# Kernel tuning notes

Measured on AMD Instinct MI355X. Metric: run time of the kernel, lower is better.

Reference implementation:

```python
import jax, jax.numpy as jnp
import numpy as np

NUM_DEPTH_BINS = 64
EPS = 1e-8


def bilinear_grid_sample(feats, grid):
    """torch.nn.functional.grid_sample, mode='bilinear', padding_mode='zeros',
    align_corners=False.  feats: [N, C, H, W]; grid: [N, Ho, Wo, 2] in [-1, 1].
    Returns [N, C, Ho, Wo]."""
    N, C, H, W = feats.shape
    x = (grid[..., 0] + 1.0) * (W * 0.5) - 0.5  # [N, Ho, Wo]
    y = (grid[..., 1] + 1.0) * (H * 0.5) - 0.5
    x0 = jnp.floor(x)
    y0 = jnp.floor(y)
    wx1 = x - x0
    wy1 = y - y0
    wx0 = 1.0 - wx1
    wy0 = 1.0 - wy1
    feats_flat = feats.reshape(N, C, H * W)

    def gather(ix, iy):
        valid = (ix >= 0) & (ix <= W - 1) & (iy >= 0) & (iy <= H - 1)
        ixc = jnp.clip(ix, 0, W - 1).astype(jnp.int32)
        iyc = jnp.clip(iy, 0, H - 1).astype(jnp.int32)
        idx = (iyc * W + ixc).reshape(N, 1, -1)  # [N,1,Ho*Wo]
        f = jnp.take_along_axis(feats_flat, idx, axis=2).reshape(N, C, *ix.shape[1:])
        return f * valid[:, None].astype(feats.dtype)

    out = (gather(x0, y0) * (wx0 * wy0)[:, None]
           + gather(x0 + 1, y0) * (wx1 * wy0)[:, None]
           + gather(x0, y0 + 1) * (wx0 * wy1)[:, None]
           + gather(x0 + 1, y0 + 1) * (wx1 * wy1)[:, None])
    return out


def _cost_volume(cur_feats, src_feats, src_extrinsics, src_Ks, cur_invK, min_depth, max_depth):
    B, K, C, H, W = src_feats.shape
    D = NUM_DEPTH_BINS
    # log-spaced depth planes, shape [B, D, 1, 1]
    ramp = jnp.linspace(0.0, 1.0, D).reshape(1, D, 1, 1).astype(cur_feats.dtype)
    depth_planes_bd11 = jnp.exp(jnp.log(min_depth) + jnp.log(max_depth / min_depth) * ramp)
    # BackprojectDepth: half-pixel-centered homogeneous pixel coords [3, N]
    xs, ys = jnp.meshgrid(jnp.arange(W, dtype=cur_feats.dtype) + 0.5,
                          jnp.arange(H, dtype=cur_feats.dtype) + 0.5)
    pix_3n = jnp.stack([xs.ravel(), ys.ravel(), jnp.ones(H * W, cur_feats.dtype)])
    cam_dirs_b3n = jnp.einsum('bij,jn->bin', cur_invK[:, :3, :3], pix_3n)
    world_bd3n = depth_planes_bd11.reshape(B, D, 1, 1) * cam_dirs_b3n[:, None]  # [B,D,3,N]
    world_bd4n = jnp.concatenate(
        [world_bd3n, jnp.ones((B, D, 1, H * W), world_bd3n.dtype)], axis=2)
    # Project3D: P = K @ extrinsics, project, perspective divide
    P_bk34 = jnp.einsum('bkij,bkjl->bkil', src_Ks, src_extrinsics)[:, :, :3]
    cam_bkd3n = jnp.einsum('bkij,bdjn->bkdin', P_bk34, world_bd4n)  # [B,K,D,3,N]
    z_bkdn = cam_bkd3n[:, :, :, 2]
    pix_bkd2n = cam_bkd3n[:, :, :, :2] / (z_bkdn[:, :, :, None] + EPS)
    # uv = 2 * pix * (1/W, 1/H) - 1
    u = 2.0 * pix_bkd2n[:, :, :, 0] / W - 1.0
    v = 2.0 * pix_bkd2n[:, :, :, 1] / H - 1.0
    grid = jnp.stack([u, v], axis=-1).reshape(B * K, D * H, W, 2)
    warped = bilinear_grid_sample(src_feats.reshape(B * K, C, H, W), grid)
    warped = warped.reshape(B, K, C, D, H, W)
    mask = (z_bkdn > 0).astype(cur_feats.dtype).reshape(B, K, D, H, W)
    # channel dot product with current features, masked, summed over views
    dots_bkdhw = jnp.einsum('bkcdhw,bchw->bkdhw', warped, cur_feats) * mask
    cost_volume_bdhw = dots_bkdhw.sum(axis=1)
    return cost_volume_bdhw


def setup_inputs() -> dict:
    key = jax.random.key(0)
    B, K, C, H, W = 1, 7, 16, 96, 128
    k1, k2 = jax.random.split(key)
    cur_feats = jax.random.normal(k1, (B, C, H, W), jnp.float32)
    src_feats = jax.random.normal(k2, (B, K, C, H, W), jnp.float32)
    rng = np.random.default_rng(0)
    fx = 0.8 * W
    Kmat = np.array([[fx, 0, W / 2, 0], [0, fx, H / 2, 0],
                     [0, 0, 1, 0], [0, 0, 0, 1]], np.float32)

    def small_pose():
        aa = rng.normal(size=3) * 0.05
        th = np.linalg.norm(aa)
        ax = aa / (th + 1e-12)
        Kx = np.array([[0, -ax[2], ax[1]], [ax[2], 0, -ax[0]], [-ax[1], ax[0], 0]])
        R = np.eye(3) + np.sin(th) * Kx + (1 - np.cos(th)) * (Kx @ Kx)
        T = np.eye(4, dtype=np.float64)
        T[:3, :3] = R
        T[:3, 3] = rng.normal(size=3) * 0.08
        return T

    src_extrinsics = np.stack([[small_pose() for _ in range(K)] for _ in range(B)])
    src_poses = np.linalg.inv(src_extrinsics)
    return {
        'cur_feats': cur_feats,
        'src_feats': src_feats,
        'src_extrinsics': jnp.asarray(src_extrinsics, jnp.float32),
        'src_poses': jnp.asarray(src_poses, jnp.float32),
        'src_Ks': jnp.asarray(np.broadcast_to(Kmat, (B, K, 4, 4)).copy()),
        'cur_invK': jnp.asarray(np.broadcast_to(np.linalg.inv(Kmat), (B, 4, 4)).astype(np.float32).copy()),
        'min_depth': jnp.full((B, 1, 1, 1), 0.25, jnp.float32),
        'max_depth': jnp.full((B, 1, 1, 1), 5.0, jnp.float32),
    }


def reference(cur_feats, src_feats, src_extrinsics, src_poses, src_Ks, cur_invK, min_depth, max_depth):
    del src_poses  # unused, matching the original (del src_poses)
    return _cost_volume(cur_feats, src_feats, src_extrinsics, src_Ks, cur_invK, min_depth, max_depth)
```

## Files before the change

kernel.cpp:

```cpp
#include <hip/hip_runtime.h>

#define CV_H 96
#define CV_W 128
#define CV_C 16
#define CV_K 7
#define CV_D 64
#define CV_EPS 1e-8f
#define CV_HW (CV_H * CV_W)

typedef _Float16 v2h __attribute__((ext_vector_type(2)));
typedef _Float16 v8h __attribute__((ext_vector_type(8)));

#if __has_builtin(__builtin_amdgcn_fdot2)
#define FDOT2(a, b, c) __builtin_amdgcn_fdot2((a), (b), (c), false)
#else
#define FDOT2(a, b, c) ((float)(a)[0] * (float)(b)[0] + (float)(a)[1] * (float)(b)[1] + (c))
#endif

__global__ __launch_bounds__(256) void cv_prep(
    const float* __restrict__ cur, const float* __restrict__ src,
    const float* __restrict__ extr, const float* __restrict__ Ks,
    const float* __restrict__ invK, const float* __restrict__ minD,
    const float* __restrict__ maxD,
    float* __restrict__ depths, float* __restrict__ M,
    _Float16* __restrict__ srcT, _Float16* __restrict__ curT) {
    const int b = blockIdx.x;
    if (b == (CV_K + 1) * CV_H) {
        int t = threadIdx.x;
        if (t < CV_D) {
            float mn = minD[0], mx = maxD[0];
            float ramp = (float)t * (1.0f / (CV_D - 1));
            depths[t] = expf(logf(mn) + logf(mx / mn) * ramp);
        }
        if (t < CV_K) {
            const float* Km = Ks + t * 16;
            const float* E  = extr + t * 16;
            float P[3][4];
            for (int i = 0; i < 3; ++i)
                for (int j = 0; j < 4; ++j) {
                    float s = 0.f;
                    for (int l = 0; l < 4; ++l) s += Km[i * 4 + l] * E[l * 4 + j];
                    P[i][j] = s;
                }
            float* Mk = M + t * 12;
            for (int i = 0; i < 3; ++i)
                for (int j = 0; j < 3; ++j) {
                    float s = 0.f;
                    for (int l = 0; l < 3; ++l) s += P[i][l] * invK[l * 4 + j];
                    Mk[i * 3 + j] = s;
                }
            for (int i = 0; i < 3; ++i) Mk[9 + i] = P[i][3];
        }
        return;
    }
    const int g = b / CV_H;
    const int h = b % CV_H;
    const float* rowBase = (g < CV_K) ? (src + (size_t)g * CV_C * CV_HW + h * CV_W)
                                      : (cur + h * CV_W);
    __shared__ float lds[CV_C][CV_W + 2];
    const int t = threadIdx.x;
#pragma unroll
    for (int i = 0; i < 2; ++i) {
        int f  = t + i * 256;
        int c  = f >> 5;
        int w4 = (f & 31) << 2;
        float4 v = *(const float4*)(rowBase + (size_t)c * CV_HW + w4);
        lds[c][w4 + 0] = v.x; lds[c][w4 + 1] = v.y;
        lds[c][w4 + 2] = v.z; lds[c][w4 + 3] = v.w;
    }
    __syncthreads();
    const int p  = t >> 1;
    const int cb = (t & 1) << 3;
    v8h o;
#pragma unroll
    for (int j = 0; j < 8; ++j) o[j] = (_Float16)lds[cb + j][p];
    _Float16* dst = (g < CV_K)
        ? (srcT + ((size_t)g * CV_HW + h * CV_W + p) * CV_C + cb)
        : (curT + ((size_t)h * CV_W + p) * CV_C + cb);
    *(v8h*)dst = o;
}

__device__ __forceinline__ float dot16h(v8h a0, v8h a1, v8h b0, v8h b1) {
    const v2h* pa0 = (const v2h*)&a0; const v2h* pb0 = (const v2h*)&b0;
    const v2h* pa1 = (const v2h*)&a1; const v2h* pb1 = (const v2h*)&b1;
    float s = 0.f;
#pragma unroll
    for (int i = 0; i < 4; ++i) s = FDOT2(pa0[i], pb0[i], s);
#pragma unroll
    for (int i = 0; i < 4; ++i) s = FDOT2(pa1[i], pb1[i], s);
    return s;
}

__global__ __launch_bounds__(256, 4) void cv_main(
    const _Float16* __restrict__ srcT,
    const _Float16* __restrict__ curT,
    const float* __restrict__ depths,
    const float* __restrict__ Mg,
    float* __restrict__ out) {
    const int bx = blockIdx.x;
    const int wb = bx & 15;
    const int hb = (bx >> 4) % 12;
    const int db = bx / 192;
    const int wx = threadIdx.x & 7;
    const int hy = (threadIdx.x >> 3) & 7;
    const int dd = threadIdx.x >> 6;
    const int w = wb * 8 + wx;
    const int h = hb * 8 + hy;
    const int d = db * 4 + dd;

    const float px = w + 0.5f;
    const float py = h + 0.5f;
    const float depth = depths[d];

    const v8h* cp = (const v8h*)(curT + (h * CV_W + w) * CV_C);
    const v8h c0 = cp[0], c1 = cp[1];

    float acc = 0.f;
#pragma unroll
    for (int k = 0; k < CV_K; ++k) {
        const float* Mk = Mg + k * 12;
        float qx = Mk[0] * px + Mk[1] * py + Mk[2];
        float qy = Mk[3] * px + Mk[4] * py + Mk[5];
        float qz = Mk[6] * px + Mk[7] * py + Mk[8];
        float cx = depth * qx + Mk[9];
        float cy = depth * qy + Mk[10];
        float cz = depth * qz + Mk[11];
        float valid = (cz > 0.f) ? 1.f : 0.f;
        float inv = 1.0f / (fabsf(cz) + CV_EPS);
        float x = fminf(fmaxf(cx * inv - 0.5f, -4.0f), (float)(CV_W + 3));
        float y = fminf(fmaxf(cy * inv - 0.5f, -4.0f), (float)(CV_H + 3));
        float xf = floorf(x), yf = floorf(y);
        float wx1 = x - xf, wy1 = y - yf;
        float wx0 = 1.f - wx1, wy0 = 1.f - wy1;
        int x0 = (int)xf, y0 = (int)yf;
        int x1 = x0 + 1, y1 = y0 + 1;
        bool vx0 = (unsigned)x0 < (unsigned)CV_W;
        bool vx1 = (unsigned)x1 < (unsigned)CV_W;
        bool vy0 = (unsigned)y0 < (unsigned)CV_H;
        bool vy1 = (unsigned)y1 < (unsigned)CV_H;
        int cx0 = min(max(x0, 0), CV_W - 1);
        int cx1 = min(max(x1, 0), CV_W - 1);
        int cy0 = min(max(y0, 0), CV_H - 1);
        int cy1 = min(max(y1, 0), CV_H - 1);
        const v8h* base = (const v8h*)srcT + (size_t)k * (CV_HW * 2);
        const v8h* r0 = base + cy0 * (CV_W * 2);
        const v8h* r1 = base + cy1 * (CV_W * 2);
        v8h a00 = r0[cx0 * 2], b00 = r0[cx0 * 2 + 1];
        v8h a10 = r0[cx1 * 2], b10 = r0[cx1 * 2 + 1];
        v8h a01 = r1[cx0 * 2], b01 = r1[cx0 * 2 + 1];
        v8h a11 = r1[cx1 * 2], b11 = r1[cx1 * 2 + 1];
        float w00 = (vx0 && vy0) ? wx0 * wy0 : 0.f;
        float w10 = (vx1 && vy0) ? wx1 * wy0 : 0.f;
        float w01 = (vx0 && vy1) ? wx0 * wy1 : 0.f;
        float w11 = (vx1 && vy1) ? wx1 * wy1 : 0.f;
        float s = w00 * dot16h(a00, b00, c0, c1)
                + w10 * dot16h(a10, b10, c0, c1)
                + w01 * dot16h(a01, b01, c0, c1)
                + w11 * dot16h(a11, b11, c0, c1);
        acc = fmaf(valid, s, acc);
    }
    out[(d * CV_H + h) * CV_W + w] = acc;
}

extern "C" void kernel_launch(void* const* d_in, const int* in_sizes, int n_in,
                              void* d_out, int out_size, void* d_ws, size_t ws_size,
                              hipStream_t stream) {
    const float* cur_feats = (const float*)d_in[0];
    const float* src_feats = (const float*)d_in[1];
    const float* extr      = (const float*)d_in[2];
    const float* Ks        = (const float*)d_in[4];
    const float* invK      = (const float*)d_in[5];
    const float* minD      = (const float*)d_in[6];
    const float* maxD      = (const float*)d_in[7];
    float* out = (float*)d_out;

    float* wsf    = (float*)d_ws;
    float* depths = wsf;
    float* M      = wsf + 64;
    _Float16* srcT = (_Float16*)(wsf + 256);
    _Float16* curT = srcT + CV_K * CV_HW * CV_C;

    cv_prep<<<(CV_K + 1) * CV_H + 1, 256, 0, stream>>>(
        cur_feats, src_feats, extr, Ks, invK, minD, maxD, depths, M, srcT, curT);

    cv_main<<<CV_D / 4 * (CV_H / 8) * (CV_W / 8), 256, 0, stream>>>(
        srcT, curT, depths, M, out);
}
```

Before: 34.30 us.

## Fuse prep and main kernels with a grid-wide atomic barrier

Merges the transpose/convert prep kernel and the cost-volume kernel into one 768-block launch. Blocks first transpose their feature rows to fp16, then wait on a global atomic counter barrier before sampling. Each thread now handles 4 depth planes so projection terms are reused across them. Each block also recomputes the projection matrices and depth values itself. The aim is to drop a kernel launch gap, at the cost of a memset, a spin barrier that needs all 768 blocks co-resident, and redundant per-block setup.

```diff
diff --git a/kernel.cpp b/kernel.cpp
--- a/kernel.cpp
+++ b/kernel.cpp
@@ -7,6 +7,7 @@
 #define CV_D 64
 #define CV_EPS 1e-8f
 #define CV_HW (CV_H * CV_W)
+#define CV_NBLK 768
 
 typedef _Float16 v2h __attribute__((ext_vector_type(2)));
 typedef _Float16 v8h __attribute__((ext_vector_type(8)));
@@ -16,69 +17,6 @@
 #else
 #define FDOT2(a, b, c) ((float)(a)[0] * (float)(b)[0] + (float)(a)[1] * (float)(b)[1] + (c))
 #endif
-
-__global__ __launch_bounds__(256) void cv_prep(
-    const float* __restrict__ cur, const float* __restrict__ src,
-    const float* __restrict__ extr, const float* __restrict__ Ks,
-    const float* __restrict__ invK, const float* __restrict__ minD,
-    const float* __restrict__ maxD,
-    float* __restrict__ depths, float* __restrict__ M,
-    _Float16* __restrict__ srcT, _Float16* __restrict__ curT) {
-    const int b = blockIdx.x;
-    if (b == (CV_K + 1) * CV_H) {
-        int t = threadIdx.x;
-        if (t < CV_D) {
-            float mn = minD[0], mx = maxD[0];
-            float ramp = (float)t * (1.0f / (CV_D - 1));
-            depths[t] = expf(logf(mn) + logf(mx / mn) * ramp);
-        }
-        if (t < CV_K) {
-            const float* Km = Ks + t * 16;
-            const float* E  = extr + t * 16;
-            float P[3][4];
-            for (int i = 0; i < 3; ++i)
-                for (int j = 0; j < 4; ++j) {
-                    float s = 0.f;
-                    for (int l = 0; l < 4; ++l) s += Km[i * 4 + l] * E[l * 4 + j];
-                    P[i][j] = s;
-                }
-            float* Mk = M + t * 12;
-            for (int i = 0; i < 3; ++i)
-                for (int j = 0; j < 3; ++j) {
-                    float s = 0.f;
-                    for (int l = 0; l < 3; ++l) s += P[i][l] * invK[l * 4 + j];
-                    Mk[i * 3 + j] = s;
-                }
-            for (int i = 0; i < 3; ++i) Mk[9 + i] = P[i][3];
-        }
-        return;
-    }
-    const int g = b / CV_H;
-    const int h = b % CV_H;
-    const float* rowBase = (g < CV_K) ? (src + (size_t)g * CV_C * CV_HW + h * CV_W)
-                                      : (cur + h * CV_W);
-    __shared__ float lds[CV_C][CV_W + 2];
-    const int t = threadIdx.x;
-#pragma unroll
-    for (int i = 0; i < 2; ++i) {
-        int f  = t + i * 256;
-        int c  = f >> 5;
-        int w4 = (f & 31) << 2;
-        float4 v = *(const float4*)(rowBase + (size_t)c * CV_HW + w4);
-        lds[c][w4 + 0] = v.x; lds[c][w4 + 1] = v.y;
-        lds[c][w4 + 2] = v.z; lds[c][w4 + 3] = v.w;
-    }
-    __syncthreads();
-    const int p  = t >> 1;
-    const int cb = (t & 1) << 3;
-    v8h o;
-#pragma unroll
-    for (int j = 0; j < 8; ++j) o[j] = (_Float16)lds[cb + j][p];
-    _Float16* dst = (g < CV_K)
-        ? (srcT + ((size_t)g * CV_HW + h * CV_W + p) * CV_C + cb)
-        : (curT + ((size_t)h * CV_W + p) * CV_C + cb);
-    *(v8h*)dst = o;
-}
 
 __device__ __forceinline__ float dot16h(v8h a0, v8h a1, v8h b0, v8h b1) {
     const v2h* pa0 = (const v2h*)&a0; const v2h* pb0 = (const v2h*)&b0;
@@ -91,75 +29,146 @@
     return s;
 }
 
-__global__ __launch_bounds__(256, 4) void cv_main(
-    const _Float16* __restrict__ srcT,
-    const _Float16* __restrict__ curT,
-    const float* __restrict__ depths,
-    const float* __restrict__ Mg,
-    float* __restrict__ out) {
-    const int bx = blockIdx.x;
-    const int wb = bx & 15;
-    const int hb = (bx >> 4) % 12;
-    const int db = bx / 192;
-    const int wx = threadIdx.x & 7;
-    const int hy = (threadIdx.x >> 3) & 7;
-    const int dd = threadIdx.x >> 6;
-    const int w = wb * 8 + wx;
-    const int h = hb * 8 + hy;
-    const int d = db * 4 + dd;
+__global__ __launch_bounds__(256, 4) void cv_fused(
+    const float* __restrict__ cur, const float* __restrict__ src,
+    const float* __restrict__ extr, const float* __restrict__ Ks,
+    const float* __restrict__ invK, const float* __restrict__ minD,
+    const float* __restrict__ maxD,
+    _Float16* __restrict__ srcT, _Float16* __restrict__ curT,
+    unsigned* __restrict__ counter, float* __restrict__ out) {
+    const int b = blockIdx.x;
+    const int t = threadIdx.x;
+
+    __shared__ float Ml[CV_K][12];
+    __shared__ float dparams[2];
+
+    {
+        const int g = b / CV_H, h = b % CV_H;
+        const float* rowBase = (g < CV_K) ? src + (size_t)g * CV_C * CV_HW + h * CV_W
+                                          : cur + h * CV_W;
+        __shared__ float lds[CV_C][CV_W + 2];
+#pragma unroll
+        for (int i = 0; i < 2; ++i) {
+            int f = t + i * 256, c = f >> 5, w4 = (f & 31) << 2;
+            float4 v = *(const float4*)(rowBase + (size_t)c * CV_HW + w4);
+            lds[c][w4 + 0] = v.x; lds[c][w4 + 1] = v.y;
+            lds[c][w4 + 2] = v.z; lds[c][w4 + 3] = v.w;
+        }
+        __syncthreads();
+        int p = t >> 1, cb = (t & 1) << 3;
+        v8h o;
+#pragma unroll
+        for (int j = 0; j < 8; ++j) o[j] = (_Float16)lds[cb + j][p];
+        _Float16* dst = (g < CV_K)
+            ? (srcT + ((size_t)g * CV_HW + h * CV_W + p) * CV_C + cb)
+            : (curT + ((size_t)h * CV_W + p) * CV_C + cb);
+        *(v8h*)dst = o;
+    }
+
+    if (t < CV_K * 12) {
+        int k = t / 12, e = t % 12;
+        const float* Km = Ks + k * 16;
+        const float* E  = extr + k * 16;
+        float s = 0.f;
+        if (e < 9) {
+            int i = e / 3, j = e % 3;
+            for (int l = 0; l < 3; ++l) {
+                float P = 0.f;
+                for (int m = 0; m < 4; ++m) P += Km[i * 4 + m] * E[m * 4 + l];
+                s += P * invK[l * 4 + j];
+            }
+        } else {
+            int i = e - 9;
+            for (int m = 0; m < 4; ++m) s += Km[i * 4 + m] * E[m * 4 + 3];
+        }
+        Ml[k][e] = s;
+    }
+    if (t == 255) {
+        float mn = minD[0], mx = maxD[0];
+        dparams[0] = logf(mn);
+        dparams[1] = logf(mx / mn);
+    }
+
+    __syncthreads();
+    if (t == 0) {
+        __threadfence();
+        atomicAdd(counter, 1u);
+        while (atomicAdd(counter, 0u) < CV_NBLK) {
+            __builtin_amdgcn_s_sleep(2);
+        }
+        __threadfence();
+    }
+    __syncthreads();
+
+    const int wx = t & 7, hy = (t >> 3) & 7, dd = t >> 6;
+    const int rem = b % 192;
+    const int db2 = b / 192;
+    const int w = (rem & 15) * 8 + wx;
+    const int h = (rem >> 4) * 8 + hy;
+    const int dbase = db2 * 16 + dd * 4;
 
     const float px = w + 0.5f;
     const float py = h + 0.5f;
-    const float depth = depths[d];
+    const float ld = dparams[0], lr = dparams[1];
+    float dpt[4];
+#pragma unroll
+    for (int j = 0; j < 4; ++j)
+        dpt[j] = expf(ld + lr * ((float)(dbase + j) * (1.0f / 63.0f)));
 
     const v8h* cp = (const v8h*)(curT + (h * CV_W + w) * CV_C);
     const v8h c0 = cp[0], c1 = cp[1];
 
-    float acc = 0.f;
+    float acc[4] = {0.f, 0.f, 0.f, 0.f};
 #pragma unroll
     for (int k = 0; k < CV_K; ++k) {
-        const float* Mk = Mg + k * 12;
-        float qx = Mk[0] * px + Mk[1] * py + Mk[2];
-        float qy = Mk[3] * px + Mk[4] * py + Mk[5];
-        float qz = Mk[6] * px + Mk[7] * py + Mk[8];
-        float cx = depth * qx + Mk[9];
-        float cy = depth * qy + Mk[10];
-        float cz = depth * qz + Mk[11];
-        float valid = (cz > 0.f) ? 1.f : 0.f;
-        float inv = 1.0f / (fabsf(cz) + CV_EPS);
-        float x = fminf(fmaxf(cx * inv - 0.5f, -4.0f), (float)(CV_W + 3));
-        float y = fminf(fmaxf(cy * inv - 0.5f, -4.0f), (float)(CV_H + 3));
-        float xf = floorf(x), yf = floorf(y);
-        float wx1 = x - xf, wy1 = y - yf;
-        float wx0 = 1.f - wx1, wy0 = 1.f - wy1;
-        int x0 = (int)xf, y0 = (int)yf;
-        int x1 = x0 + 1, y1 = y0 + 1;
-        bool vx0 = (unsigned)x0 < (unsigned)CV_W;
-        bool vx1 = (unsigned)x1 < (unsigned)CV_W;
-        bool vy0 = (unsigned)y0 < (unsigned)CV_H;
-        bool vy1 = (unsigned)y1 < (unsigned)CV_H;
-        int cx0 = min(max(x0, 0), CV_W - 1);
-        int cx1 = min(max(x1, 0), CV_W - 1);
-        int cy0 = min(max(y0, 0), CV_H - 1);
-        int cy1 = min(max(y1, 0), CV_H - 1);
+        const float* Mk = Ml[k];
+        const float qx = Mk[0] * px + Mk[1] * py + Mk[2];
+        const float qy = Mk[3] * px + Mk[4] * py + Mk[5];
+        const float qz = Mk[6] * px + Mk[7] * py + Mk[8];
         const v8h* base = (const v8h*)srcT + (size_t)k * (CV_HW * 2);
-        const v8h* r0 = base + cy0 * (CV_W * 2);
-        const v8h* r1 = base + cy1 * (CV_W * 2);
-        v8h a00 = r0[cx0 * 2], b00 = r0[cx0 * 2 + 1];
-        v8h a10 = r0[cx1 * 2], b10 = r0[cx1 * 2 + 1];
-        v8h a01 = r1[cx0 * 2], b01 = r1[cx0 * 2 + 1];
-        v8h a11 = r1[cx1 * 2], b11 = r1[cx1 * 2 + 1];
-        float w00 = (vx0 && vy0) ? wx0 * wy0 : 0.f;
-        float w10 = (vx1 && vy0) ? wx1 * wy0 : 0.f;
-        float w01 = (vx0 && vy1) ? wx0 * wy1 : 0.f;
-        float w11 = (vx1 && vy1) ? wx1 * wy1 : 0.f;
-        float s = w00 * dot16h(a00, b00, c0, c1)
-                + w10 * dot16h(a10, b10, c0, c1)
-                + w01 * dot16h(a01, b01, c0, c1)
-                + w11 * dot16h(a11, b11, c0, c1);
-        acc = fmaf(valid, s, acc);
+#pragma unroll
+        for (int j = 0; j < 4; ++j) {
+            float depth = dpt[j];
+            float cx = depth * qx + Mk[9];
+            float cy = depth * qy + Mk[10];
+            float cz = depth * qz + Mk[11];
+            float valid = (cz > 0.f) ? 1.f : 0.f;
+            float inv = 1.0f / (fabsf(cz) + CV_EPS);
+            float x = fminf(fmaxf(cx * inv - 0.5f, -4.0f), (float)(CV_W + 3));
+            float y = fminf(fmaxf(cy * inv - 0.5f, -4.0f), (float)(CV_H + 3));
+            float xf = floorf(x), yf = floorf(y);
+            float wx1 = x - xf, wy1 = y - yf;
+            float wx0 = 1.f - wx1, wy0 = 1.f - wy1;
+            int x0 = (int)xf, y0 = (int)yf;
+            int x1 = x0 + 1, y1 = y0 + 1;
+            bool vx0 = (unsigned)x0 < (unsigned)CV_W;
+            bool vx1 = (unsigned)x1 < (unsigned)CV_W;
+            bool vy0 = (unsigned)y0 < (unsigned)CV_H;
+            bool vy1 = (unsigned)y1 < (unsigned)CV_H;
+            int cx0 = min(max(x0, 0), CV_W - 1);
+            int cx1 = min(max(x1, 0), CV_W - 1);
+            int cy0 = min(max(y0, 0), CV_H - 1);
+            int cy1 = min(max(y1, 0), CV_H - 1);
+            const v8h* r0 = base + cy0 * (CV_W * 2);
+            const v8h* r1 = base + cy1 * (CV_W * 2);
+            v8h a00 = r0[cx0 * 2], b00 = r0[cx0 * 2 + 1];
+            v8h a10 = r0[cx1 * 2], b10 = r0[cx1 * 2 + 1];
+            v8h a01 = r1[cx0 * 2], b01 = r1[cx0 * 2 + 1];
+            v8h a11 = r1[cx1 * 2], b11 = r1[cx1 * 2 + 1];
+            float w00 = (vx0 && vy0) ? wx0 * wy0 : 0.f;
+            float w10 = (vx1 && vy0) ? wx1 * wy0 : 0.f;
+            float w01 = (vx0 && vy1) ? wx0 * wy1 : 0.f;
+            float w11 = (vx1 && vy1) ? wx1 * wy1 : 0.f;
+            float s = w00 * dot16h(a00, b00, c0, c1)
+                    + w10 * dot16h(a10, b10, c0, c1)
+                    + w01 * dot16h(a01, b01, c0, c1)
+                    + w11 * dot16h(a11, b11, c0, c1);
+            acc[j] = fmaf(valid, s, acc[j]);
+        }
     }
-    out[(d * CV_H + h) * CV_W + w] = acc;
+#pragma unroll
+    for (int j = 0; j < 4; ++j)
+        out[((dbase + j) * CV_H + h) * CV_W + w] = acc[j];
 }
 
 extern "C" void kernel_launch(void* const* d_in, const int* in_sizes, int n_in,
@@ -174,15 +183,12 @@
     const float* maxD      = (const float*)d_in[7];
     float* out = (float*)d_out;
 
-    float* wsf    = (float*)d_ws;
-    float* depths = wsf;
-    float* M      = wsf + 64;
-    _Float16* srcT = (_Float16*)(wsf + 256);
-    _Float16* curT = srcT + CV_K * CV_HW * CV_C;
+    unsigned* counter = (unsigned*)d_ws;
+    _Float16* srcT = (_Float16*)((char*)d_ws + 1024);
+    _Float16* curT = srcT + (size_t)CV_K * CV_HW * CV_C;
 
-    cv_prep<<<(CV_K + 1) * CV_H + 1, 256, 0, stream>>>(
-        cur_feats, src_feats, extr, Ks, invK, minD, maxD, depths, M, srcT, curT);
+    hipMemsetAsync(d_ws, 0, 4, stream);
 
-    cv_main<<<CV_D / 4 * (CV_H / 8) * (CV_W / 8), 256, 0, stream>>>(
-        srcT, curT, depths, M, out);
+    cv_fused<<<CV_NBLK, 256, 0, stream>>>(cur_feats, src_feats, extr, Ks, invK,
+                                          minD, maxD, srcT, curT, counter, out);
 }
```

New measurement: 93.08 us. 171% more time.

## Process four depth planes per thread in cost-volume kernel

Applied to the files above, without the earlier changes.

Each thread now handles four depth bins instead of one. The per-pixel projection terms (qx, qy, qz and the translation) and the current-feature load are computed once and reused across the four depths, and the grid shrinks fourfold. The reciprocal switches to the hardware rcp builtin, and the launch-bounds occupancy hint drops from 4 to 3 to allow more registers. The trade-off is fewer blocks (768) and higher register pressure, which may reduce latency hiding for the gather loads.

```diff
diff --git a/kernel.cpp b/kernel.cpp
--- a/kernel.cpp
+++ b/kernel.cpp
@@ -91,75 +91,82 @@
     return s;
 }
 
-__global__ __launch_bounds__(256, 4) void cv_main(
+__global__ __launch_bounds__(256, 3) void cv_main(
     const _Float16* __restrict__ srcT,
     const _Float16* __restrict__ curT,
     const float* __restrict__ depths,
     const float* __restrict__ Mg,
     float* __restrict__ out) {
-    const int bx = blockIdx.x;
-    const int wb = bx & 15;
-    const int hb = (bx >> 4) % 12;
-    const int db = bx / 192;
-    const int wx = threadIdx.x & 7;
-    const int hy = (threadIdx.x >> 3) & 7;
-    const int dd = threadIdx.x >> 6;
-    const int w = wb * 8 + wx;
-    const int h = hb * 8 + hy;
-    const int d = db * 4 + dd;
+    const int bx  = blockIdx.x;
+    const int rem = bx % 192;
+    const int db2 = bx / 192;
+    const int t   = threadIdx.x;
+    const int wx = t & 7, hy = (t >> 3) & 7, dd = t >> 6;
+    const int w = (rem & 15) * 8 + wx;
+    const int h = (rem >> 4) * 8 + hy;
+    const int dbase = db2 * 16 + dd * 4;
 
     const float px = w + 0.5f;
     const float py = h + 0.5f;
-    const float depth = depths[d];
+    float dpt[4];
+#pragma unroll
+    for (int j = 0; j < 4; ++j) dpt[j] = depths[dbase + j];
 
     const v8h* cp = (const v8h*)(curT + (h * CV_W + w) * CV_C);
     const v8h c0 = cp[0], c1 = cp[1];
 
-    float acc = 0.f;
+    float acc[4] = {0.f, 0.f, 0.f, 0.f};
 #pragma unroll
     for (int k = 0; k < CV_K; ++k) {
         const float* Mk = Mg + k * 12;
-        float qx = Mk[0] * px + Mk[1] * py + Mk[2];
-        float qy = Mk[3] * px + Mk[4] * py + Mk[5];
-        float qz = Mk[6] * px + Mk[7] * py + Mk[8];
-        float cx = depth * qx + Mk[9];
-        float cy = depth * qy + Mk[10];
-        float cz = depth * qz + Mk[11];
-        float valid = (cz > 0.f) ? 1.f : 0.f;
-        float inv = 1.0f / (fabsf(cz) + CV_EPS);
-        float x = fminf(fmaxf(cx * inv - 0.5f, -4.0f), (float)(CV_W + 3));
-        float y = fminf(fmaxf(cy * inv - 0.5f, -4.0f), (float)(CV_H + 3));
-        float xf = floorf(x), yf = floorf(y);
-        float wx1 = x - xf, wy1 = y - yf;
-        float wx0 = 1.f - wx1, wy0 = 1.f - wy1;
-        int x0 = (int)xf, y0 = (int)yf;
-        int x1 = x0 + 1, y1 = y0 + 1;
-        bool vx0 = (unsigned)x0 < (unsigned)CV_W;
-        bool vx1 = (unsigned)x1 < (unsigned)CV_W;
-        bool vy0 = (unsigned)y0 < (unsigned)CV_H;
-        bool vy1 = (unsigned)y1 < (unsigned)CV_H;
-        int cx0 = min(max(x0, 0), CV_W - 1);
-        int cx1 = min(max(x1, 0), CV_W - 1);
-        int cy0 = min(max(y0, 0), CV_H - 1);
-        int cy1 = min(max(y1, 0), CV_H - 1);
+        const float qx = Mk[0] * px + Mk[1] * py + Mk[2];
+        const float qy = Mk[3] * px + Mk[4] * py + Mk[5];
+        const float qz = Mk[6] * px + Mk[7] * py + Mk[8];
+        const float bxk = Mk[9], byk = Mk[10], bzk = Mk[11];
         const v8h* base = (const v8h*)srcT + (size_t)k * (CV_HW * 2);
-        const v8h* r0 = base + cy0 * (CV_W * 2);
-        const v8h* r1 = base + cy1 * (CV_W * 2);
-        v8h a00 = r0[cx0 * 2], b00 = r0[cx0 * 2 + 1];
-        v8h a10 = r0[cx1 * 2], b10 = r0[cx1 * 2 + 1];
-        v8h a01 = r1[cx0 * 2], b01 = r1[cx0 * 2 + 1];
-        v8h a11 = r1[cx1 * 2], b11 = r1[cx1 * 2 + 1];
-        float w00 = (vx0 && vy0) ? wx0 * wy0 : 0.f;
-        float w10 = (vx1 && vy0) ? wx1 * wy0 : 0.f;
-        float w01 = (vx0 && vy1) ? wx0 * wy1 : 0.f;
-        float w11 = (vx1 && vy1) ? wx1 * wy1 : 0.f;
-        float s = w00 * dot16h(a00, b00, c0, c1)
-                + w10 * dot16h(a10, b10, c0, c1)
-                + w01 * dot16h(a01, b01, c0, c1)
-                + w11 * dot16h(a11, b11, c0, c1);
-        acc = fmaf(valid, s, acc);
+#pragma unroll
+        for (int j = 0; j < 4; ++j) {
+            float depth = dpt[j];
+            float cx = fmaf(depth, qx, bxk);
+            float cy = fmaf(depth, qy, byk);
+            float cz = fmaf(depth, qz, bzk);
+            float valid = (cz > 0.f) ? 1.f : 0.f;
+            float inv = __builtin_amdgcn_rcpf(fabsf(cz) + CV_EPS);
+            float x = fminf(fmaxf(fmaf(cx, inv, -0.5f), -4.0f), (float)(CV_W + 3));
+            float y = fminf(fmaxf(fmaf(cy, inv, -0.5f), -4.0f), (float)(CV_H + 3));
+            float xf = floorf(x), yf = floorf(y);
+            float wx1 = x - xf, wy1 = y - yf;
+            float wx0 = 1.f - wx1, wy0 = 1.f - wy1;
+            int x0 = (int)xf, y0 = (int)yf;
+            int x1 = x0 + 1, y1 = y0 + 1;
+            bool vx0 = (unsigned)x0 < (unsigned)CV_W;
+            bool vx1 = (unsigned)x1 < (unsigned)CV_W;
+            bool vy0 = (unsigned)y0 < (unsigned)CV_H;
+            bool vy1 = (unsigned)y1 < (unsigned)CV_H;
+            int cx0 = min(max(x0, 0), CV_W - 1);
+            int cx1 = min(max(x1, 0), CV_W - 1);
+            int cy0 = min(max(y0, 0), CV_H - 1);
+            int cy1 = min(max(y1, 0), CV_H - 1);
+            const v8h* r0 = base + cy0 * (CV_W * 2);
+            const v8h* r1 = base + cy1 * (CV_W * 2);
+            v8h a00 = r0[cx0 * 2], b00 = r0[cx0 * 2 + 1];
+            v8h a10 = r0[cx1 * 2], b10 = r0[cx1 * 2 + 1];
+            v8h a01 = r1[cx0 * 2], b01 = r1[cx0 * 2 + 1];
+            v8h a11 = r1[cx1 * 2], b11 = r1[cx1 * 2 + 1];
+            float w00 = (vx0 && vy0) ? wx0 * wy0 : 0.f;
+            float w10 = (vx1 && vy0) ? wx1 * wy0 : 0.f;
+            float w01 = (vx0 && vy1) ? wx0 * wy1 : 0.f;
+            float w11 = (vx1 && vy1) ? wx1 * wy1 : 0.f;
+            float s = w00 * dot16h(a00, b00, c0, c1)
+                    + w10 * dot16h(a10, b10, c0, c1)
+                    + w01 * dot16h(a01, b01, c0, c1)
+                    + w11 * dot16h(a11, b11, c0, c1);
+            acc[j] = fmaf(valid, s, acc[j]);
+        }
     }
-    out[(d * CV_H + h) * CV_W + w] = acc;
+#pragma unroll
+    for (int j = 0; j < 4; ++j)
+        out[((dbase + j) * CV_H + h) * CV_W + w] = acc[j];
 }
 
 extern "C" void kernel_launch(void* const* d_in, const int* in_sizes, int n_in,
@@ -178,11 +185,11 @@
     float* depths = wsf;
     float* M      = wsf + 64;
     _Float16* srcT = (_Float16*)(wsf + 256);
-    _Float16* curT = srcT + CV_K * CV_HW * CV_C;
+    _Float16* curT = srcT + (size_t)CV_K * CV_HW * CV_C;
 
     cv_prep<<<(CV_K + 1) * CV_H + 1, 256, 0, stream>>>(
         cur_feats, src_feats, extr, Ks, invK, minD, maxD, depths, M, srcT, curT);
 
-    cv_main<<<CV_D / 4 * (CV_H / 8) * (CV_W / 8), 256, 0, stream>>>(
+    cv_main<<<(CV_D / 16) * (CV_H / 8) * (CV_W / 8), 256, 0, stream>>>(
         srcT, curT, depths, M, out);
 }
```

After: 33.07 us. 3.6% less time.
